# Kernel tuning notes

Measured on AMD Instinct MI355X. Metric: run time of the kernel, lower is better.

The kernel has to match this reference:

```python
import jax, jax.numpy as jnp
import numpy as np

C = 128
NUM_GROUPS = 32
EPS = 1e-6


def setup_inputs() -> dict:
    key = jax.random.key(0)
    ks = jax.random.split(key, 6)
    B, H, W = 8, 64, 64
    x = jax.random.normal(ks[0], (B, C, H, W), dtype=jnp.float32)
    # 1x1 conv weights stored as [out_c, in_c] (kernel spatial dims are 1)
    fan_avg = C  # fan_in == fan_out == C for 1x1 conv
    bound = np.sqrt(3.0 / fan_avg)
    wq = jax.random.uniform(ks[1], (C, C), jnp.float32, -bound, bound)
    wk = jax.random.uniform(ks[2], (C, C), jnp.float32, -bound, bound)
    wv = jax.random.uniform(ks[3], (C, C), jnp.float32, -bound, bound)
    # proj_out has init_scale=0.0 -> near-zero init; use tiny random instead to test math
    wo = jax.random.uniform(ks[4], (C, C), jnp.float32, -bound, bound) * 1e-3
    bq = jnp.zeros((C,), jnp.float32)
    bk = jnp.zeros((C,), jnp.float32)
    bv = jnp.zeros((C,), jnp.float32)
    bo = jnp.zeros((C,), jnp.float32)
    gamma = jnp.ones((C,), jnp.float32)
    beta = jnp.zeros((C,), jnp.float32)
    return {"x": x, "gamma": gamma, "beta": beta,
            "wq": wq, "bq": bq, "wk": wk, "bk": bk,
            "wv": wv, "bv": bv, "wo": wo, "bo": bo}


def _group_norm(x, gamma, beta):
    B, Ch, H, W = x.shape
    g = NUM_GROUPS
    xg = x.reshape(B, g, Ch // g, H, W)
    mean = jnp.mean(xg, axis=(2, 3, 4), keepdims=True)
    var = jnp.var(xg, axis=(2, 3, 4), keepdims=True)
    xn = ((xg - mean) * jax.lax.rsqrt(var + EPS)).reshape(B, Ch, H, W)
    return xn * gamma[None, :, None, None] + beta[None, :, None, None]


def _conv1x1(x, w, b):
    # x: [B,C,H,W], w: [O,C], b: [O]
    return jnp.einsum('bchw,oc->bohw', x, w) + b[None, :, None, None]


def reference(x, gamma, beta, wq, bq, wk, bk, wv, bv, wo, bo):
    B, Ch, H, W = x.shape
    n = H * W
    h = _group_norm(x, gamma, beta)
    q = _conv1x1(h, wq, bq).reshape(B, Ch, n)
    k = _conv1x1(h, wk, bk).reshape(B, Ch, n)
    v = _conv1x1(h, wv, bv).reshape(B, Ch, n)
    # attn[b, i, j] = sum_c q[b,c,i] * k[b,c,j] / sqrt(C)
    attn = jnp.einsum('bci,bcj->bij', q, k) * (float(Ch) ** -0.5)
    attn = jax.nn.softmax(attn, axis=-1)
    # h[b,c,i] = sum_j v[b,c,j] * attn[b,i,j]
    out = jnp.einsum('bcj,bij->bci', v, attn).reshape(B, Ch, H, W)
    out = _conv1x1(out, wo, bo)
    return x + out
```

## Files before the change

### kernel.cpp

```cpp
#include <hip/hip_runtime.h>


typedef float f32x4 __attribute__((ext_vector_type(4)));
typedef float f32x2 __attribute__((ext_vector_type(2)));
typedef short short8 __attribute__((ext_vector_type(8)));
typedef _Float16 half8 __attribute__((ext_vector_type(8)));
typedef _Float16 half2t __attribute__((ext_vector_type(2)));
typedef unsigned short ush;
typedef unsigned short ush4 __attribute__((ext_vector_type(4)));
typedef unsigned int uint4t __attribute__((ext_vector_type(4)));
typedef int int8v __attribute__((ext_vector_type(8)));
typedef unsigned long long ull;

union V8U {
  uint4t h[2];
  int8v v;
};

__device__ __forceinline__ ush f2bf(float f) {
  unsigned u = __builtin_bit_cast(unsigned, f);
  u = (u + 0x7FFFu + ((u >> 16) & 1u)) >> 16;
  return (ush)u;
}
__device__ __forceinline__ void async16(const void* g, void* l) {
  __builtin_amdgcn_global_load_lds(
      (const __attribute__((address_space(1))) unsigned int*)g,
      (__attribute__((address_space(3))) unsigned int*)l, 16, 0, 0);
}

__global__ __launch_bounds__(256) void gn_stats_kernel(
    const float* __restrict__ x, const float* __restrict__ gamma,
    const float* __restrict__ beta, const float* __restrict__ wo,
    const float* __restrict__ wq, const float* __restrict__ wk,
    const float* __restrict__ wv, float* __restrict__ scale_c,
    float* __restrict__ shift_c, ush* __restrict__ wobh,
    ush* __restrict__ wqh, ush* __restrict__ wkh, ush* __restrict__ wvh) {
  int bg = blockIdx.x;
  int b = bg >> 5, g = bg & 31;
  int tid = threadIdx.x;
  if (bg < 64) {
    int m = bg >> 4;
    int v4 = ((bg & 15) * 256 + tid) * 4;
    const float* src = m == 0 ? wo : (m == 1 ? wq : (m == 2 ? wk : wv));
    float4 w4 = *(const float4*)(src + v4);
    ush4 pk;
    pk.x = __builtin_bit_cast(ush, (_Float16)w4.x);
    pk.y = __builtin_bit_cast(ush, (_Float16)w4.y);
    pk.z = __builtin_bit_cast(ush, (_Float16)w4.z);
    pk.w = __builtin_bit_cast(ush, (_Float16)w4.w);
    ush* dst = m == 0 ? wobh : (m == 1 ? wqh : (m == 2 ? wkh : wvh));
    *(ush4*)(dst + v4) = pk;
  }
  const float4* base = (const float4*)(x + (size_t)bg * 16384);
  float s = 0.f, sq = 0.f;
#pragma unroll
  for (int p = 0; p < 16; ++p) {
    float4 v = base[p * 256 + tid];
    s += (v.x + v.y) + (v.z + v.w);
    sq += (v.x * v.x + v.y * v.y) + (v.z * v.z + v.w * v.w);
  }
#pragma unroll
  for (int off = 32; off > 0; off >>= 1) {
    s += __shfl_down(s, off);
    sq += __shfl_down(sq, off);
  }
  __shared__ float rs[4], rq[4], mv[2];
  int w = tid >> 6, lane = tid & 63;
  if (lane == 0) { rs[w] = s; rq[w] = sq; }
  __syncthreads();
  if (tid == 0) {
    float S = (rs[0] + rs[1]) + (rs[2] + rs[3]);
    float Q = (rq[0] + rq[1]) + (rq[2] + rq[3]);
    float mean = S * (1.f / 16384.f);
    float var = Q * (1.f / 16384.f) - mean * mean;
    mv[0] = mean;
    mv[1] = rsqrtf(var + 1e-6f);
  }
  __syncthreads();
  if (tid < 4) {
    int c = (g << 2) + tid;
    float sc = mv[1] * gamma[c];
    scale_c[(b << 7) + c] = sc;
    shift_c[(b << 7) + c] = beta[c] - mv[0] * sc;
  }
}

__global__ __launch_bounds__(256) void qkv_kernel(
    const float* __restrict__ x, const float* __restrict__ scale_c,
    const float* __restrict__ shift_c, const ush* __restrict__ wqh,
    const ush* __restrict__ wkh, const ush* __restrict__ wvh,
    const float* __restrict__ bq, const float* __restrict__ bk,
    const float* __restrict__ bv, char* __restrict__ Qt8,
    char* __restrict__ Kt8, _Float16* __restrict__ Vh) {
  __shared__ __align__(16) ush hs[64 * 136];
  __shared__ __align__(16) ush wol[128 * 136];
  char* hs8 = (char*)hs;
  int bx = blockIdx.x;
  int type = bx >> 9;
  int rb = bx & 511;
  int b = rb >> 6, i0 = (rb & 63) << 6;
  int tid = threadIdx.x;
  int w = tid >> 6, lane = tid & 63, ln15 = lane & 15, quad = lane >> 4;

#pragma unroll
  for (int p = 0; p < 8; ++p) {
    int id = p * 256 + tid;
    int i = id & 63;
    int g8 = id >> 6;
    int c0 = g8 << 2;
    const float* xp = x + (((size_t)((b << 7) + c0)) << 12) + i0 + i;
    float h0 = xp[0] * scale_c[(b << 7) + c0] + shift_c[(b << 7) + c0];
    float h1 = xp[(size_t)1 << 12] * scale_c[(b << 7) + c0 + 1] +
               shift_c[(b << 7) + c0 + 1];
    float h2 = xp[(size_t)2 << 12] * scale_c[(b << 7) + c0 + 2] +
               shift_c[(b << 7) + c0 + 2];
    float h3 = xp[(size_t)3 << 12] * scale_c[(b << 7) + c0 + 3] +
               shift_c[(b << 7) + c0 + 3];
    uint2 pk2;
    pk2.x = __builtin_bit_cast(unsigned, __builtin_amdgcn_cvt_pkrtz(h0, h1));
    pk2.y = __builtin_bit_cast(unsigned, __builtin_amdgcn_cvt_pkrtz(h2, h3));
    int pg = g8 ^ ((i & 15) << 1);
    *(uint2*)(hs8 + i * 272 + pg * 8) = pk2;
  }
  const ush* Wb = type == 0 ? wqh : (type == 1 ? wkh : wvh);
#pragma unroll
  for (int p = 0; p < 8; ++p) {
    int cid = p * 256 + tid;
    int o = cid >> 4, ch = (cid & 15) << 3;
    *(uint4t*)&wol[o * 136 + ch] = *(const uint4t*)(Wb + (o << 7) + ch);
  }
  __syncthreads();

#define HS_FRAG(row, dc)                                     \
  __builtin_bit_cast(half8, *(const short8*)(hs8 + (row) * 272 + \
      (((((dc)*4 + quad)) ^ ((row)&15)) << 4)))
#define W_FRAG(o, dc)                                         \
  __builtin_bit_cast(half8, *(const short8*)&wol[(o)*136 + (dc)*32 + quad * 8])

  if (type < 2) {
    f32x4 acc[8] = {};
    int hrow = w * 16 + ln15;
#pragma unroll
    for (int dc = 0; dc < 4; ++dc) {
      half8 af = HS_FRAG(hrow, dc);
#pragma unroll
      for (int nb = 0; nb < 8; ++nb) {
        half8 bf = W_FRAG(nb * 16 + ln15, dc);
        acc[nb] = __builtin_amdgcn_mfma_f32_16x16x32_f16(af, bf, acc[nb], 0, 0, 0);
      }
    }
    const float* bias = type == 0 ? bq : bk;
    char* dst8 = type == 0 ? Qt8 : Kt8;
    __syncthreads();
#pragma unroll
    for (int nb = 0; nb < 8; ++nb) {
      int o = nb * 16 + ln15;
      float bi = bias[o];
      float v0 = acc[nb][0] + bi, v1 = acc[nb][1] + bi;
      float v2 = acc[nb][2] + bi, v3 = acc[nb][3] + bi;
      if (type == 0) {
        v0 *= 0.12751742f; v1 *= 0.12751742f;
        v2 *= 0.12751742f; v3 *= 0.12751742f;
      }
      unsigned u = (unsigned)__builtin_amdgcn_cvt_pk_fp8_f32(v0, v1, 0, false);
      u = (unsigned)__builtin_amdgcn_cvt_pk_fp8_f32(v2, v3, (int)u, true);
      int rbase = (w * 16 + quad * 4) * 144 + o;
      hs8[rbase] = (char)(u & 0xffu);
      hs8[rbase + 144] = (char)((u >> 8) & 0xffu);
      hs8[rbase + 288] = (char)((u >> 16) & 0xffu);
      hs8[rbase + 432] = (char)(u >> 24);
    }
    __syncthreads();
    int i = tid >> 2, seg = tid & 3;
    uint4 d0 = *(const uint4*)(hs8 + i * 144 + seg * 32);
    uint4 d1 = *(const uint4*)(hs8 + i * 144 + seg * 32 + 16);
    char* drow = dst8 + (((size_t)((b << 12) + i0 + i)) << 7) + seg * 32;
    *(uint4*)drow = d0;
    *(uint4*)(drow + 16) = d1;
  } else {
    f32x4 acc[8] = {};
    int hrow = w * 16 + ln15;
#pragma unroll
    for (int dc = 0; dc < 4; ++dc) {
      half8 bf = HS_FRAG(hrow, dc);
#pragma unroll
      for (int mb = 0; mb < 8; ++mb) {
        half8 af = W_FRAG(mb * 16 + ln15, dc);
        acc[mb] = __builtin_amdgcn_mfma_f32_16x16x32_f16(af, bf, acc[mb], 0, 0, 0);
      }
    }
#pragma unroll
    for (int mb = 0; mb < 8; ++mb) {
#pragma unroll
      for (int r = 0; r < 4; ++r) {
        int o = mb * 16 + quad * 4 + r;
        float val = acc[mb][r] + bv[o];
        Vh[(((size_t)((b << 7) + o)) << 12) + i0 + w * 16 + ln15] = (_Float16)val;
      }
    }
  }
#undef HS_FRAG
#undef W_FRAG
}

__global__ __launch_bounds__(256, 2) void attn_kernel(
    const char* __restrict__ Qt8, const char* __restrict__ Kt8,
    const _Float16* __restrict__ Vh, char* __restrict__ po,
    float* __restrict__ lw) {
  __shared__ __align__(16) char ksb[2][4096];
  __shared__ __align__(16) _Float16 vsb[2][4096];
  int bx = blockIdx.x;
  int b = bx & 7, qt = (bx >> 3) & 15, ksid = bx >> 7;
  int tid = threadIdx.x;
  int w = tid >> 6, lane = tid & 63, ln15 = lane & 15, quad = lane >> 4;
  int qbase = (qt << 8) + (w << 6);
  int j0 = ksid << 10;

  int8v qf[4];
#pragma unroll
  for (int ih = 0; ih < 4; ++ih) {
    const char* qrow =
        Qt8 + (((size_t)((b << 12) + qbase + ih * 16 + ln15)) << 7) + quad * 32;
    V8U u;
    u.h[0] = *(const uint4t*)(qrow);
    u.h[1] = *(const uint4t*)(qrow + 16);
    qf[ih] = u.v;
  }

  int kj = (w << 3) + (lane >> 3);
  int kh = (kj & 3) | (((kj >> 3) & 1) << 2);
  int kg = (lane & 7) ^ kh;
  const char* ksrc = Kt8 + (((size_t)((b << 12) + j0 + kj)) << 7) + (kg << 4);
  int d0r = (w << 5) + (lane >> 2);
  int d1r = d0r + 16;
  int vg0 = (lane & 3) ^ (((d0r >> 1) + (d0r >> 3)) & 3);
  int vg1 = (lane & 3) ^ (((d1r >> 1) + (d1r >> 3)) & 3);
  const _Float16* vsrc0 =
      Vh + (((size_t)((b << 7) + d0r)) << 12) + j0 + (vg0 << 3);
  const _Float16* vsrc1 =
      Vh + (((size_t)((b << 7) + d1r)) << 12) + j0 + (vg1 << 3);
  char* kdA = &ksb[0][0] + (w << 10);
  char* kdB = &ksb[1][0] + (w << 10);
  char* vdA0 = (char*)&vsb[0][0] + ((w * 2 + 0) << 10);
  char* vdA1 = (char*)&vsb[0][0] + ((w * 2 + 1) << 10);
  char* vdB0 = (char*)&vsb[1][0] + ((w * 2 + 0) << 10);
  char* vdB1 = (char*)&vsb[1][0] + ((w * 2 + 1) << 10);

  async16(ksrc, kdA);
  async16(vsrc0, vdA0);
  async16(vsrc1, vdA1);
  __syncthreads();

  f32x4 O[4][8] = {};
  float lsum[4] = {0.f, 0.f, 0.f, 0.f};
  const f32x4 SINIT = {-7.2134752f, -7.2134752f, -7.2134752f, -7.2134752f};
  int r0 = ((ln15 >> 2) << 3) + (ln15 & 3), r1 = r0 + 4;
  int hr = (ln15 & 3) | (((ln15 >> 2) & 1) << 2);
  int g0 = ((2 * quad) ^ hr) << 4;
  int g1 = ((2 * quad + 1) ^ hr) << 4;

  for (int jt = 0; jt < 32; ++jt) {
    int buf = jt & 1;
    if (jt + 1 < 32) {
      ksrc += 4096;
      vsrc0 += 32;
      vsrc1 += 32;
      if (buf == 0) {
        async16(ksrc, kdB);
        async16(vsrc0, vdB0);
        async16(vsrc1, vdB1);
      } else {
        async16(ksrc, kdA);
        async16(vsrc0, vdA0);
        async16(vsrc1, vdA1);
      }
    }
    const char* kb = &ksb[buf][0];
    const char* vb = (const char*)&vsb[buf][0];

    V8U ka, kc;
    ka.h[0] = *(const uint4t*)(kb + r0 * 128 + g0);
    ka.h[1] = *(const uint4t*)(kb + r0 * 128 + g1);
    kc.h[0] = *(const uint4t*)(kb + r1 * 128 + g0);
    kc.h[1] = *(const uint4t*)(kb + r1 * 128 + g1);
    f32x4 S[4][2];
#pragma unroll
    for (int ih = 0; ih < 4; ++ih) {
      S[ih][0] = __builtin_amdgcn_mfma_scale_f32_16x16x128_f8f6f4(
          ka.v, qf[ih], SINIT, 0, 0, 0, 0x7F7F7F7F, 0, 0x7F7F7F7F);
      S[ih][1] = __builtin_amdgcn_mfma_scale_f32_16x16x128_f8f6f4(
          kc.v, qf[ih], SINIT, 0, 0, 0, 0x7F7F7F7F, 0, 0x7F7F7F7F);
    }

    half8 pf[4];
#pragma unroll
    for (int ih = 0; ih < 4; ++ih) {
      float p0 = __builtin_amdgcn_exp2f(S[ih][0][0]);
      float p1 = __builtin_amdgcn_exp2f(S[ih][0][1]);
      float p2 = __builtin_amdgcn_exp2f(S[ih][0][2]);
      float p3 = __builtin_amdgcn_exp2f(S[ih][0][3]);
      float p4 = __builtin_amdgcn_exp2f(S[ih][1][0]);
      float p5 = __builtin_amdgcn_exp2f(S[ih][1][1]);
      float p6 = __builtin_amdgcn_exp2f(S[ih][1][2]);
      float p7 = __builtin_amdgcn_exp2f(S[ih][1][3]);
      lsum[ih] += ((p0 + p1) + (p2 + p3)) + ((p4 + p5) + (p6 + p7));
      uint4t pw;
      pw.x = __builtin_bit_cast(unsigned, __builtin_amdgcn_cvt_pkrtz(p0, p1));
      pw.y = __builtin_bit_cast(unsigned, __builtin_amdgcn_cvt_pkrtz(p2, p3));
      pw.z = __builtin_bit_cast(unsigned, __builtin_amdgcn_cvt_pkrtz(p4, p5));
      pw.w = __builtin_bit_cast(unsigned, __builtin_amdgcn_cvt_pkrtz(p6, p7));
      pf[ih] = __builtin_bit_cast(half8, pw);
    }
#pragma unroll
    for (int nb = 0; nb < 8; ++nb) {
      int d = nb * 16 + ln15;
      int sd = ((d >> 1) + (d >> 3)) & 3;
      half8 vf = *(const half8*)(vb + d * 64 + ((quad ^ sd) << 4));
#pragma unroll
      for (int ih = 0; ih < 4; ++ih)
        O[ih][nb] = __builtin_amdgcn_mfma_f32_16x16x32_f16(vf, pf[ih], O[ih][nb], 0, 0, 0);
    }
    __syncthreads();
  }

#pragma unroll
  for (int ih = 0; ih < 4; ++ih) {
    float l = lsum[ih];
    l += __shfl_xor(l, 16);
    l += __shfl_xor(l, 32);
    if (quad == 0) lw[(ksid << 15) + (b << 12) + qbase + ih * 16 + ln15] = l;
    int i = qbase + ih * 16 + ln15;
    size_t rowb = (((size_t)((ksid * 8 + b)) << 12) + i) << 7;
#pragma unroll
    for (int nb = 0; nb < 8; ++nb) {
      unsigned u = (unsigned)__builtin_amdgcn_cvt_pk_fp8_f32(
          O[ih][nb][0], O[ih][nb][1], 0, false);
      u = (unsigned)__builtin_amdgcn_cvt_pk_fp8_f32(
          O[ih][nb][2], O[ih][nb][3], (int)u, true);
      *(unsigned*)(po + rowb + nb * 16 + quad * 4) = u;
    }
  }
}

__global__ __launch_bounds__(256) void proj_kernel(
    const float* __restrict__ x, const char* __restrict__ po,
    const float* __restrict__ lw, const ush* __restrict__ wobh,
    const float* __restrict__ bo, float* __restrict__ out) {
  int bx = blockIdx.x;
  int oh = bx & 1;
  int bi = bx >> 1;
  int b = bi >> 6, i0 = (bi & 63) << 6;
  int tid = threadIdx.x;
  int w = tid >> 6, lane = tid & 63, ln15 = lane & 15, quad = lane >> 4;
  int i = i0 + w * 16 + ln15;
  float rl = 0.f;
#pragma unroll
  for (int s = 0; s < 4; ++s) rl += lw[(s << 15) + (b << 12) + i];
  float rinv = 1.f / rl;

  f32x4 acc[4] = {};
#pragma unroll
  for (int dc = 0; dc < 4; ++dc) {
    size_t base = ((size_t)i << 7) + dc * 32 + quad * 8;
    float vs0 = 0.f, vs1 = 0.f, vs2 = 0.f, vs3 = 0.f;
    float vs4 = 0.f, vs5 = 0.f, vs6 = 0.f, vs7 = 0.f;
#pragma unroll
    for (int s = 0; s < 4; ++s) {
      ull pv = *(const ull*)(po + (((size_t)(s * 8 + b)) << 19) + base);
      int lo = (int)(unsigned)pv, hi = (int)(unsigned)(pv >> 32);
      f32x2 a0 = __builtin_amdgcn_cvt_pk_f32_fp8(lo, false);
      f32x2 a1 = __builtin_amdgcn_cvt_pk_f32_fp8(lo, true);
      f32x2 a2 = __builtin_amdgcn_cvt_pk_f32_fp8(hi, false);
      f32x2 a3 = __builtin_amdgcn_cvt_pk_f32_fp8(hi, true);
      vs0 += a0.x; vs1 += a0.y; vs2 += a1.x; vs3 += a1.y;
      vs4 += a2.x; vs5 += a2.y; vs6 += a3.x; vs7 += a3.y;
    }
    uint4t pw;
    pw.x = __builtin_bit_cast(unsigned,
                              __builtin_amdgcn_cvt_pkrtz(vs0 * rinv, vs1 * rinv));
    pw.y = __builtin_bit_cast(unsigned,
                              __builtin_amdgcn_cvt_pkrtz(vs2 * rinv, vs3 * rinv));
    pw.z = __builtin_bit_cast(unsigned,
                              __builtin_amdgcn_cvt_pkrtz(vs4 * rinv, vs5 * rinv));
    pw.w = __builtin_bit_cast(unsigned,
                              __builtin_amdgcn_cvt_pkrtz(vs6 * rinv, vs7 * rinv));
    half8 bfv = __builtin_bit_cast(half8, pw);
#pragma unroll
    for (int mb = 0; mb < 4; ++mb) {
      half8 af = *(const half8*)&wobh[(((oh * 4 + mb) * 16 + ln15) << 7) +
                                      dc * 32 + quad * 8];
      acc[mb] = __builtin_amdgcn_mfma_f32_16x16x32_f16(af, bfv, acc[mb], 0, 0, 0);
    }
  }
#pragma unroll
  for (int mb = 0; mb < 4; ++mb) {
#pragma unroll
    for (int r = 0; r < 4; ++r) {
      int o = (oh * 4 + mb) * 16 + quad * 4 + r;
      size_t idx = (((size_t)(b << 7) + o) << 12) + i;
      out[idx] = x[idx] + acc[mb][r] + bo[o];
    }
  }
}

extern "C" void kernel_launch(void* const* d_in, const int* in_sizes, int n_in,
                              void* d_out, int out_size, void* d_ws,
                              size_t ws_size, hipStream_t stream) {
  const float* x = (const float*)d_in[0];
  const float* gamma = (const float*)d_in[1];
  const float* beta = (const float*)d_in[2];
  const float* wq = (const float*)d_in[3];
  const float* bq = (const float*)d_in[4];
  const float* wk = (const float*)d_in[5];
  const float* bk = (const float*)d_in[6];
  const float* wv = (const float*)d_in[7];
  const float* bv = (const float*)d_in[8];
  const float* wo = (const float*)d_in[9];
  const float* bo = (const float*)d_in[10];
  float* out = (float*)d_out;

  const size_t NE = (size_t)8 * 4096 * 128;
  char* Qt8 = (char*)d_ws;
  char* Kt8 = Qt8 + NE;
  _Float16* Vh = (_Float16*)(Kt8 + NE);
  char* po = (char*)(Vh + NE);
  float* lwp = (float*)(po + 4 * NE);
  float* scale_c = lwp + 4 * 32768;
  float* shift_c = scale_c + 1024;
  ush* wobh = (ush*)(shift_c + 1024);
  ush* wqh = wobh + 16384;
  ush* wkh = wqh + 16384;
  ush* wvh = wkh + 16384;

  gn_stats_kernel<<<256, 256, 0, stream>>>(x, gamma, beta, wo, wq, wk, wv,
                                           scale_c, shift_c, wobh, wqh, wkh,
                                           wvh);
  qkv_kernel<<<1536, 256, 0, stream>>>(x, scale_c, shift_c, wqh, wkh, wvh, bq,
                                       bk, bv, Qt8, Kt8, Vh);
  attn_kernel<<<512, 256, 0, stream>>>(Qt8, Kt8, Vh, po, lwp);
  proj_kernel<<<1024, 256, 0, stream>>>(x, po, lwp, wobh, bo, out);
}
```

Baseline: 178.4 us.

## Fuse four kernels into one persistent kernel with grid-wide atomic barriers

Merges the group-norm stats, QKV projection, attention and output projection kernels into a single 512-block persistent kernel, separated by software grid barriers built on atomic counters. The aim is to remove three kernel launch gaps and tail effects between stages. The QKV stage now does Q, K and V per block sequentially, reusing the normalized tile in LDS instead of recomputing it in three separate blocks. The proj stage now covers all output channels per block rather than splitting them over two blocks. This relies on all 512 blocks being co-resident (launch bounds of 2 blocks per CU) and adds a memset plus spin-wait overhead.

```diff
diff --git a/kernel.cpp b/kernel.cpp
--- a/kernel.cpp
+++ b/kernel.cpp
@@ -5,7 +5,6 @@
 typedef float f32x2 __attribute__((ext_vector_type(2)));
 typedef short short8 __attribute__((ext_vector_type(8)));
 typedef _Float16 half8 __attribute__((ext_vector_type(8)));
-typedef _Float16 half2t __attribute__((ext_vector_type(2)));
 typedef unsigned short ush;
 typedef unsigned short ush4 __attribute__((ext_vector_type(4)));
 typedef unsigned int uint4t __attribute__((ext_vector_type(4)));
@@ -17,30 +16,83 @@
   int8v v;
 };
 
-__device__ __forceinline__ ush f2bf(float f) {
-  unsigned u = __builtin_bit_cast(unsigned, f);
-  u = (u + 0x7FFFu + ((u >> 16) & 1u)) >> 16;
-  return (ush)u;
-}
 __device__ __forceinline__ void async16(const void* g, void* l) {
   __builtin_amdgcn_global_load_lds(
       (const __attribute__((address_space(1))) unsigned int*)g,
       (__attribute__((address_space(3))) unsigned int*)l, 16, 0, 0);
 }
 
-__global__ __launch_bounds__(256) void gn_stats_kernel(
+__device__ __forceinline__ void gbar(unsigned* cnt, int tid) {
+  __threadfence();
+  __syncthreads();
+  if (tid == 0) {
+    __hip_atomic_fetch_add(cnt, 1u, __ATOMIC_RELEASE,
+                           __HIP_MEMORY_SCOPE_AGENT);
+    int spins = 0;
+    while (__hip_atomic_load(cnt, __ATOMIC_ACQUIRE,
+                             __HIP_MEMORY_SCOPE_AGENT) < 512u &&
+           ++spins < (1 << 22)) {
+      __builtin_amdgcn_s_sleep(8);
+    }
+  }
+  __syncthreads();
+  __threadfence();
+}
+
+__global__ __launch_bounds__(256, 2) void fused_kernel(
     const float* __restrict__ x, const float* __restrict__ gamma,
-    const float* __restrict__ beta, const float* __restrict__ wo,
-    const float* __restrict__ wq, const float* __restrict__ wk,
-    const float* __restrict__ wv, float* __restrict__ scale_c,
-    float* __restrict__ shift_c, ush* __restrict__ wobh,
-    ush* __restrict__ wqh, ush* __restrict__ wkh, ush* __restrict__ wvh) {
-  int bg = blockIdx.x;
-  int b = bg >> 5, g = bg & 31;
-  int tid = threadIdx.x;
-  if (bg < 64) {
-    int m = bg >> 4;
-    int v4 = ((bg & 15) * 256 + tid) * 4;
+    const float* __restrict__ beta, const float* __restrict__ wq,
+    const float* __restrict__ bq, const float* __restrict__ wk,
+    const float* __restrict__ bk, const float* __restrict__ wv,
+    const float* __restrict__ bv, const float* __restrict__ wo,
+    const float* __restrict__ bo, float* __restrict__ out,
+    char* __restrict__ Qt8, char* __restrict__ Kt8, _Float16* __restrict__ Vh,
+    char* __restrict__ po, float* __restrict__ lw,
+    float* __restrict__ scale_c, float* __restrict__ shift_c,
+    ush* __restrict__ wobh, ush* __restrict__ wqh, ush* __restrict__ wkh,
+    ush* __restrict__ wvh, unsigned* __restrict__ bar) {
+  __shared__ __align__(16) char smem[52224];
+  int bx = blockIdx.x, tid = threadIdx.x;
+  int w = tid >> 6, lane = tid & 63, ln15 = lane & 15, quad = lane >> 4;
+
+  if (bx < 256) {
+    int bg = bx, b = bg >> 5, g = bg & 31;
+    float* rs = (float*)smem;
+    float* rq = rs + 4;
+    float* mv = rq + 4;
+    const float4* base = (const float4*)(x + (size_t)bg * 16384);
+    float s = 0.f, sq = 0.f;
+#pragma unroll
+    for (int p = 0; p < 16; ++p) {
+      float4 v = base[p * 256 + tid];
+      s += (v.x + v.y) + (v.z + v.w);
+      sq += (v.x * v.x + v.y * v.y) + (v.z * v.z + v.w * v.w);
+    }
+#pragma unroll
+    for (int off = 32; off > 0; off >>= 1) {
+      s += __shfl_down(s, off);
+      sq += __shfl_down(sq, off);
+    }
+    if (lane == 0) { rs[w] = s; rq[w] = sq; }
+    __syncthreads();
+    if (tid == 0) {
+      float S = (rs[0] + rs[1]) + (rs[2] + rs[3]);
+      float Q = (rq[0] + rq[1]) + (rq[2] + rq[3]);
+      float mean = S * (1.f / 16384.f);
+      float var = Q * (1.f / 16384.f) - mean * mean;
+      mv[0] = mean;
+      mv[1] = rsqrtf(var + 1e-6f);
+    }
+    __syncthreads();
+    if (tid < 4) {
+      int c = (g << 2) + tid;
+      float sc = mv[1] * gamma[c];
+      scale_c[(b << 7) + c] = sc;
+      shift_c[(b << 7) + c] = beta[c] - mv[0] * sc;
+    }
+  } else if (bx < 320) {
+    int u = bx - 256, m = u >> 4;
+    int v4 = ((u & 15) * 256 + tid) * 4;
     const float* src = m == 0 ? wo : (m == 1 ? wq : (m == 2 ? wk : wv));
     float4 w4 = *(const float4*)(src + v4);
     ush4 pk;
@@ -51,142 +103,303 @@
     ush* dst = m == 0 ? wobh : (m == 1 ? wqh : (m == 2 ? wkh : wvh));
     *(ush4*)(dst + v4) = pk;
   }
-  const float4* base = (const float4*)(x + (size_t)bg * 16384);
-  float s = 0.f, sq = 0.f;
-#pragma unroll
-  for (int p = 0; p < 16; ++p) {
-    float4 v = base[p * 256 + tid];
-    s += (v.x + v.y) + (v.z + v.w);
-    sq += (v.x * v.x + v.y * v.y) + (v.z * v.z + v.w * v.w);
-  }
-#pragma unroll
-  for (int off = 32; off > 0; off >>= 1) {
-    s += __shfl_down(s, off);
-    sq += __shfl_down(sq, off);
-  }
-  __shared__ float rs[4], rq[4], mv[2];
-  int w = tid >> 6, lane = tid & 63;
-  if (lane == 0) { rs[w] = s; rq[w] = sq; }
-  __syncthreads();
-  if (tid == 0) {
-    float S = (rs[0] + rs[1]) + (rs[2] + rs[3]);
-    float Q = (rq[0] + rq[1]) + (rq[2] + rq[3]);
-    float mean = S * (1.f / 16384.f);
-    float var = Q * (1.f / 16384.f) - mean * mean;
-    mv[0] = mean;
-    mv[1] = rsqrtf(var + 1e-6f);
-  }
-  __syncthreads();
-  if (tid < 4) {
-    int c = (g << 2) + tid;
-    float sc = mv[1] * gamma[c];
-    scale_c[(b << 7) + c] = sc;
-    shift_c[(b << 7) + c] = beta[c] - mv[0] * sc;
-  }
-}
-
-__global__ __launch_bounds__(256) void qkv_kernel(
-    const float* __restrict__ x, const float* __restrict__ scale_c,
-    const float* __restrict__ shift_c, const ush* __restrict__ wqh,
-    const ush* __restrict__ wkh, const ush* __restrict__ wvh,
-    const float* __restrict__ bq, const float* __restrict__ bk,
-    const float* __restrict__ bv, char* __restrict__ Qt8,
-    char* __restrict__ Kt8, _Float16* __restrict__ Vh) {
-  __shared__ __align__(16) ush hs[64 * 136];
-  __shared__ __align__(16) ush wol[128 * 136];
-  char* hs8 = (char*)hs;
-  int bx = blockIdx.x;
-  int type = bx >> 9;
-  int rb = bx & 511;
-  int b = rb >> 6, i0 = (rb & 63) << 6;
-  int tid = threadIdx.x;
-  int w = tid >> 6, lane = tid & 63, ln15 = lane & 15, quad = lane >> 4;
-
-#pragma unroll
-  for (int p = 0; p < 8; ++p) {
-    int id = p * 256 + tid;
-    int i = id & 63;
-    int g8 = id >> 6;
-    int c0 = g8 << 2;
-    const float* xp = x + (((size_t)((b << 7) + c0)) << 12) + i0 + i;
-    float h0 = xp[0] * scale_c[(b << 7) + c0] + shift_c[(b << 7) + c0];
-    float h1 = xp[(size_t)1 << 12] * scale_c[(b << 7) + c0 + 1] +
-               shift_c[(b << 7) + c0 + 1];
-    float h2 = xp[(size_t)2 << 12] * scale_c[(b << 7) + c0 + 2] +
-               shift_c[(b << 7) + c0 + 2];
-    float h3 = xp[(size_t)3 << 12] * scale_c[(b << 7) + c0 + 3] +
-               shift_c[(b << 7) + c0 + 3];
-    uint2 pk2;
-    pk2.x = __builtin_bit_cast(unsigned, __builtin_amdgcn_cvt_pkrtz(h0, h1));
-    pk2.y = __builtin_bit_cast(unsigned, __builtin_amdgcn_cvt_pkrtz(h2, h3));
-    int pg = g8 ^ ((i & 15) << 1);
-    *(uint2*)(hs8 + i * 272 + pg * 8) = pk2;
-  }
-  const ush* Wb = type == 0 ? wqh : (type == 1 ? wkh : wvh);
-#pragma unroll
-  for (int p = 0; p < 8; ++p) {
-    int cid = p * 256 + tid;
-    int o = cid >> 4, ch = (cid & 15) << 3;
-    *(uint4t*)&wol[o * 136 + ch] = *(const uint4t*)(Wb + (o << 7) + ch);
-  }
-  __syncthreads();
-
-#define HS_FRAG(row, dc)                                     \
+  gbar(bar + 0, tid);
+
+  {
+    int b = bx >> 6, i0 = (bx & 63) << 6;
+    char* hs8 = smem;
+    ush* wol = (ush*)(smem + 17408);
+    char* wolb = (char*)wol;
+
+#pragma unroll
+    for (int p = 0; p < 8; ++p) {
+      int id = p * 256 + tid;
+      int i = id & 63;
+      int g8 = id >> 6;
+      int c0 = g8 << 2;
+      const float* xp = x + (((size_t)((b << 7) + c0)) << 12) + i0 + i;
+      float h0 = xp[0] * scale_c[(b << 7) + c0] + shift_c[(b << 7) + c0];
+      float h1 = xp[(size_t)1 << 12] * scale_c[(b << 7) + c0 + 1] +
+                 shift_c[(b << 7) + c0 + 1];
+      float h2 = xp[(size_t)2 << 12] * scale_c[(b << 7) + c0 + 2] +
+                 shift_c[(b << 7) + c0 + 2];
+      float h3 = xp[(size_t)3 << 12] * scale_c[(b << 7) + c0 + 3] +
+                 shift_c[(b << 7) + c0 + 3];
+      uint2 pk2;
+      pk2.x = __builtin_bit_cast(unsigned, __builtin_amdgcn_cvt_pkrtz(h0, h1));
+      pk2.y = __builtin_bit_cast(unsigned, __builtin_amdgcn_cvt_pkrtz(h2, h3));
+      int pg = g8 ^ ((i & 15) << 1);
+      *(uint2*)(hs8 + i * 272 + pg * 8) = pk2;
+    }
+#pragma unroll
+    for (int p = 0; p < 8; ++p) {
+      int cid = p * 256 + tid;
+      int o = cid >> 4, ch = (cid & 15) << 3;
+      *(uint4t*)&wol[o * 136 + ch] = *(const uint4t*)(wqh + (o << 7) + ch);
+    }
+    __syncthreads();
+
+#define HS_FRAG(row, dc)                                         \
   __builtin_bit_cast(half8, *(const short8*)(hs8 + (row) * 272 + \
       (((((dc)*4 + quad)) ^ ((row)&15)) << 4)))
-#define W_FRAG(o, dc)                                         \
+#define W_FRAG(o, dc)                                            \
   __builtin_bit_cast(half8, *(const short8*)&wol[(o)*136 + (dc)*32 + quad * 8])
-
-  if (type < 2) {
+    int hrow = w * 16 + ln15;
+
+#pragma unroll 1
+    for (int type = 0; type < 2; ++type) {
+      f32x4 acc[8] = {};
+#pragma unroll
+      for (int dc = 0; dc < 4; ++dc) {
+        half8 af = HS_FRAG(hrow, dc);
+#pragma unroll
+        for (int nb = 0; nb < 8; ++nb) {
+          half8 bf = W_FRAG(nb * 16 + ln15, dc);
+          acc[nb] = __builtin_amdgcn_mfma_f32_16x16x32_f16(af, bf, acc[nb], 0, 0, 0);
+        }
+      }
+      const float* bias = type == 0 ? bq : bk;
+      char* dst8 = type == 0 ? Qt8 : Kt8;
+      __syncthreads();
+#pragma unroll
+      for (int nb = 0; nb < 8; ++nb) {
+        int o = nb * 16 + ln15;
+        float bi = bias[o];
+        float v0 = acc[nb][0] + bi, v1 = acc[nb][1] + bi;
+        float v2 = acc[nb][2] + bi, v3 = acc[nb][3] + bi;
+        if (type == 0) {
+          v0 *= 0.12751742f; v1 *= 0.12751742f;
+          v2 *= 0.12751742f; v3 *= 0.12751742f;
+        }
+        unsigned u = (unsigned)__builtin_amdgcn_cvt_pk_fp8_f32(v0, v1, 0, false);
+        u = (unsigned)__builtin_amdgcn_cvt_pk_fp8_f32(v2, v3, (int)u, true);
+        int rbase = (w * 16 + quad * 4) * 144 + o;
+        wolb[rbase] = (char)(u & 0xffu);
+        wolb[rbase + 144] = (char)((u >> 8) & 0xffu);
+        wolb[rbase + 288] = (char)((u >> 16) & 0xffu);
+        wolb[rbase + 432] = (char)(u >> 24);
+      }
+      __syncthreads();
+      {
+        int i = tid >> 2, seg = tid & 3;
+        uint4 d0 = *(const uint4*)(wolb + i * 144 + seg * 32);
+        uint4 d1 = *(const uint4*)(wolb + i * 144 + seg * 32 + 16);
+        char* drow = dst8 + (((size_t)((b << 12) + i0 + i)) << 7) + seg * 32;
+        *(uint4*)drow = d0;
+        *(uint4*)(drow + 16) = d1;
+      }
+      __syncthreads();
+      const ush* Wn = type == 0 ? wkh : wvh;
+#pragma unroll
+      for (int p = 0; p < 8; ++p) {
+        int cid = p * 256 + tid;
+        int o = cid >> 4, ch = (cid & 15) << 3;
+        *(uint4t*)&wol[o * 136 + ch] = *(const uint4t*)(Wn + (o << 7) + ch);
+      }
+      __syncthreads();
+    }
+    {
+      f32x4 acc[8] = {};
+#pragma unroll
+      for (int dc = 0; dc < 4; ++dc) {
+        half8 bf = HS_FRAG(hrow, dc);
+#pragma unroll
+        for (int mb = 0; mb < 8; ++mb) {
+          half8 af = W_FRAG(mb * 16 + ln15, dc);
+          acc[mb] = __builtin_amdgcn_mfma_f32_16x16x32_f16(af, bf, acc[mb], 0, 0, 0);
+        }
+      }
+#pragma unroll
+      for (int mb = 0; mb < 8; ++mb) {
+#pragma unroll
+        for (int r = 0; r < 4; ++r) {
+          int o = mb * 16 + quad * 4 + r;
+          float val = acc[mb][r] + bv[o];
+          Vh[(((size_t)((b << 7) + o)) << 12) + i0 + w * 16 + ln15] =
+              (_Float16)val;
+        }
+      }
+    }
+#undef HS_FRAG
+#undef W_FRAG
+  }
+  gbar(bar + 1, tid);
+
+  {
+    int b = bx & 7, qt = (bx >> 3) & 15, ksid = bx >> 7;
+    int qbase = (qt << 8) + (w << 6);
+    int j0 = ksid << 10;
+    char* ksbp = smem;
+    char* vsbp = smem + 8192;
+
+    int8v qf[4];
+#pragma unroll
+    for (int ih = 0; ih < 4; ++ih) {
+      const char* qrow = Qt8 +
+                         (((size_t)((b << 12) + qbase + ih * 16 + ln15)) << 7) +
+                         quad * 32;
+      V8U u;
+      u.h[0] = *(const uint4t*)(qrow);
+      u.h[1] = *(const uint4t*)(qrow + 16);
+      qf[ih] = u.v;
+    }
+
+    int kj = (w << 3) + (lane >> 3);
+    int kh = (kj & 3) | (((kj >> 3) & 1) << 2);
+    int kg = (lane & 7) ^ kh;
+    const char* ksrc = Kt8 + (((size_t)((b << 12) + j0 + kj)) << 7) + (kg << 4);
+    int d0r = (w << 5) + (lane >> 2);
+    int d1r = d0r + 16;
+    int vg0 = (lane & 3) ^ (((d0r >> 1) + (d0r >> 3)) & 3);
+    int vg1 = (lane & 3) ^ (((d1r >> 1) + (d1r >> 3)) & 3);
+    const _Float16* vsrc0 =
+        Vh + (((size_t)((b << 7) + d0r)) << 12) + j0 + (vg0 << 3);
+    const _Float16* vsrc1 =
+        Vh + (((size_t)((b << 7) + d1r)) << 12) + j0 + (vg1 << 3);
+    char* kdA = ksbp + (w << 10);
+    char* kdB = ksbp + 4096 + (w << 10);
+    char* vdA0 = vsbp + ((w * 2 + 0) << 10);
+    char* vdA1 = vsbp + ((w * 2 + 1) << 10);
+    char* vdB0 = vsbp + 8192 + ((w * 2 + 0) << 10);
+    char* vdB1 = vsbp + 8192 + ((w * 2 + 1) << 10);
+
+    async16(ksrc, kdA);
+    async16(vsrc0, vdA0);
+    async16(vsrc1, vdA1);
+    __syncthreads();
+
+    f32x4 O[4][8] = {};
+    float lsum[4] = {0.f, 0.f, 0.f, 0.f};
+    const f32x4 SINIT = {-7.2134752f, -7.2134752f, -7.2134752f, -7.2134752f};
+    int r0 = ((ln15 >> 2) << 3) + (ln15 & 3), r1 = r0 + 4;
+    int hr = (ln15 & 3) | (((ln15 >> 2) & 1) << 2);
+    int g0 = ((2 * quad) ^ hr) << 4;
+    int g1 = ((2 * quad + 1) ^ hr) << 4;
+
+    for (int jt = 0; jt < 32; ++jt) {
+      int buf = jt & 1;
+      if (jt + 1 < 32) {
+        ksrc += 4096;
+        vsrc0 += 32;
+        vsrc1 += 32;
+        if (buf == 0) {
+          async16(ksrc, kdB);
+          async16(vsrc0, vdB0);
+          async16(vsrc1, vdB1);
+        } else {
+          async16(ksrc, kdA);
+          async16(vsrc0, vdA0);
+          async16(vsrc1, vdA1);
+        }
+      }
+      const char* kb = ksbp + buf * 4096;
+      const char* vb = vsbp + buf * 8192;
+
+      V8U ka, kc;
+      ka.h[0] = *(const uint4t*)(kb + r0 * 128 + g0);
+      ka.h[1] = *(const uint4t*)(kb + r0 * 128 + g1);
+      kc.h[0] = *(const uint4t*)(kb + r1 * 128 + g0);
+      kc.h[1] = *(const uint4t*)(kb + r1 * 128 + g1);
+      f32x4 S[4][2];
+#pragma unroll
+      for (int ih = 0; ih < 4; ++ih) {
+        S[ih][0] = __builtin_amdgcn_mfma_scale_f32_16x16x128_f8f6f4(
+            ka.v, qf[ih], SINIT, 0, 0, 0, 0x7F7F7F7F, 0, 0x7F7F7F7F);
+        S[ih][1] = __builtin_amdgcn_mfma_scale_f32_16x16x128_f8f6f4(
+            kc.v, qf[ih], SINIT, 0, 0, 0, 0x7F7F7F7F, 0, 0x7F7F7F7F);
+      }
+
+      half8 pf[4];
+#pragma unroll
+      for (int ih = 0; ih < 4; ++ih) {
+        float p0 = __builtin_amdgcn_exp2f(S[ih][0][0]);
+        float p1 = __builtin_amdgcn_exp2f(S[ih][0][1]);
+        float p2 = __builtin_amdgcn_exp2f(S[ih][0][2]);
+        float p3 = __builtin_amdgcn_exp2f(S[ih][0][3]);
+        float p4 = __builtin_amdgcn_exp2f(S[ih][1][0]);
+        float p5 = __builtin_amdgcn_exp2f(S[ih][1][1]);
+        float p6 = __builtin_amdgcn_exp2f(S[ih][1][2]);
+        float p7 = __builtin_amdgcn_exp2f(S[ih][1][3]);
+        lsum[ih] += ((p0 + p1) + (p2 + p3)) + ((p4 + p5) + (p6 + p7));
+        uint4t pw;
+        pw.x = __builtin_bit_cast(unsigned, __builtin_amdgcn_cvt_pkrtz(p0, p1));
+        pw.y = __builtin_bit_cast(unsigned, __builtin_amdgcn_cvt_pkrtz(p2, p3));
+        pw.z = __builtin_bit_cast(unsigned, __builtin_amdgcn_cvt_pkrtz(p4, p5));
+        pw.w = __builtin_bit_cast(unsigned, __builtin_amdgcn_cvt_pkrtz(p6, p7));
+        pf[ih] = __builtin_bit_cast(half8, pw);
+      }
+#pragma unroll
+      for (int nb = 0; nb < 8; ++nb) {
+        int d = nb * 16 + ln15;
+        int sd = ((d >> 1) + (d >> 3)) & 3;
+        half8 vf = *(const half8*)(vb + d * 64 + ((quad ^ sd) << 4));
+#pragma unroll
+        for (int ih = 0; ih < 4; ++ih)
+          O[ih][nb] = __builtin_amdgcn_mfma_f32_16x16x32_f16(vf, pf[ih], O[ih][nb], 0, 0, 0);
+      }
+      __syncthreads();
+    }
+
+#pragma unroll
+    for (int ih = 0; ih < 4; ++ih) {
+      float l = lsum[ih];
+      l += __shfl_xor(l, 16);
+      l += __shfl_xor(l, 32);
+      if (quad == 0) lw[(ksid << 15) + (b << 12) + qbase + ih * 16 + ln15] = l;
+      int i = qbase + ih * 16 + ln15;
+      size_t rowb = (((size_t)((ksid * 8 + b)) << 12) + i) << 7;
+#pragma unroll
+      for (int nb = 0; nb < 8; ++nb) {
+        unsigned u = (unsigned)__builtin_amdgcn_cvt_pk_fp8_f32(
+            O[ih][nb][0], O[ih][nb][1], 0, false);
+        u = (unsigned)__builtin_amdgcn_cvt_pk_fp8_f32(
+            O[ih][nb][2], O[ih][nb][3], (int)u, true);
+        *(unsigned*)(po + rowb + nb * 16 + quad * 4) = u;
+      }
+    }
+  }
+  gbar(bar + 2, tid);
+
+  {
+    int b = bx >> 6, i0 = (bx & 63) << 6;
+    int i = i0 + w * 16 + ln15;
+    float rl = 0.f;
+#pragma unroll
+    for (int s = 0; s < 4; ++s) rl += lw[(s << 15) + (b << 12) + i];
+    float rinv = 1.f / rl;
+
     f32x4 acc[8] = {};
-    int hrow = w * 16 + ln15;
 #pragma unroll
     for (int dc = 0; dc < 4; ++dc) {
-      half8 af = HS_FRAG(hrow, dc);
-#pragma unroll
-      for (int nb = 0; nb < 8; ++nb) {
-        half8 bf = W_FRAG(nb * 16 + ln15, dc);
-        acc[nb] = __builtin_amdgcn_mfma_f32_16x16x32_f16(af, bf, acc[nb], 0, 0, 0);
-      }
-    }
-    const float* bias = type == 0 ? bq : bk;
-    char* dst8 = type == 0 ? Qt8 : Kt8;
-    __syncthreads();
-#pragma unroll
-    for (int nb = 0; nb < 8; ++nb) {
-      int o = nb * 16 + ln15;
-      float bi = bias[o];
-      float v0 = acc[nb][0] + bi, v1 = acc[nb][1] + bi;
-      float v2 = acc[nb][2] + bi, v3 = acc[nb][3] + bi;
-      if (type == 0) {
-        v0 *= 0.12751742f; v1 *= 0.12751742f;
-        v2 *= 0.12751742f; v3 *= 0.12751742f;
-      }
-      unsigned u = (unsigned)__builtin_amdgcn_cvt_pk_fp8_f32(v0, v1, 0, false);
-      u = (unsigned)__builtin_amdgcn_cvt_pk_fp8_f32(v2, v3, (int)u, true);
-      int rbase = (w * 16 + quad * 4) * 144 + o;
-      hs8[rbase] = (char)(u & 0xffu);
-      hs8[rbase + 144] = (char)((u >> 8) & 0xffu);
-      hs8[rbase + 288] = (char)((u >> 16) & 0xffu);
-      hs8[rbase + 432] = (char)(u >> 24);
-    }
-    __syncthreads();
-    int i = tid >> 2, seg = tid & 3;
-    uint4 d0 = *(const uint4*)(hs8 + i * 144 + seg * 32);
-    uint4 d1 = *(const uint4*)(hs8 + i * 144 + seg * 32 + 16);
-    char* drow = dst8 + (((size_t)((b << 12) + i0 + i)) << 7) + seg * 32;
-    *(uint4*)drow = d0;
-    *(uint4*)(drow + 16) = d1;
-  } else {
-    f32x4 acc[8] = {};
-    int hrow = w * 16 + ln15;
-#pragma unroll
-    for (int dc = 0; dc < 4; ++dc) {
-      half8 bf = HS_FRAG(hrow, dc);
+      size_t base = ((size_t)i << 7) + dc * 32 + quad * 8;
+      float vs0 = 0.f, vs1 = 0.f, vs2 = 0.f, vs3 = 0.f;
+      float vs4 = 0.f, vs5 = 0.f, vs6 = 0.f, vs7 = 0.f;
+#pragma unroll
+      for (int s = 0; s < 4; ++s) {
+        ull pv = *(const ull*)(po + (((size_t)(s * 8 + b)) << 19) + base);
+        int lo = (int)(unsigned)pv, hi = (int)(unsigned)(pv >> 32);
+        f32x2 a0 = __builtin_amdgcn_cvt_pk_f32_fp8(lo, false);
+        f32x2 a1 = __builtin_amdgcn_cvt_pk_f32_fp8(lo, true);
+        f32x2 a2 = __builtin_amdgcn_cvt_pk_f32_fp8(hi, false);
+        f32x2 a3 = __builtin_amdgcn_cvt_pk_f32_fp8(hi, true);
+        vs0 += a0.x; vs1 += a0.y; vs2 += a1.x; vs3 += a1.y;
+        vs4 += a2.x; vs5 += a2.y; vs6 += a3.x; vs7 += a3.y;
+      }
+      uint4t pw;
+      pw.x = __builtin_bit_cast(unsigned,
+                                __builtin_amdgcn_cvt_pkrtz(vs0 * rinv, vs1 * rinv));
+      pw.y = __builtin_bit_cast(unsigned,
+                                __builtin_amdgcn_cvt_pkrtz(vs2 * rinv, vs3 * rinv));
+      pw.z = __builtin_bit_cast(unsigned,
+                                __builtin_amdgcn_cvt_pkrtz(vs4 * rinv, vs5 * rinv));
+      pw.w = __builtin_bit_cast(unsigned,
+                                __builtin_amdgcn_cvt_pkrtz(vs6 * rinv, vs7 * rinv));
+      half8 bfv = __builtin_bit_cast(half8, pw);
 #pragma unroll
       for (int mb = 0; mb < 8; ++mb) {
-        half8 af = W_FRAG(mb * 16 + ln15, dc);
-        acc[mb] = __builtin_amdgcn_mfma_f32_16x16x32_f16(af, bf, acc[mb], 0, 0, 0);
+        half8 af = *(const half8*)&wobh[((mb * 16 + ln15) << 7) + dc * 32 +
+                                        quad * 8];
+        acc[mb] = __builtin_amdgcn_mfma_f32_16x16x32_f16(af, bfv, acc[mb], 0, 0, 0);
       }
     }
 #pragma unroll
@@ -194,211 +407,9 @@
 #pragma unroll
       for (int r = 0; r < 4; ++r) {
         int o = mb * 16 + quad * 4 + r;
-        float val = acc[mb][r] + bv[o];
-        Vh[(((size_t)((b << 7) + o)) << 12) + i0 + w * 16 + ln15] = (_Float16)val;
-      }
-    }
-  }
-#undef HS_FRAG
-#undef W_FRAG
-}
-
-__global__ __launch_bounds__(256, 2) void attn_kernel(
-    const char* __restrict__ Qt8, const char* __restrict__ Kt8,
-    const _Float16* __restrict__ Vh, char* __restrict__ po,
-    float* __restrict__ lw) {
-  __shared__ __align__(16) char ksb[2][4096];
-  __shared__ __align__(16) _Float16 vsb[2][4096];
-  int bx = blockIdx.x;
-  int b = bx & 7, qt = (bx >> 3) & 15, ksid = bx >> 7;
-  int tid = threadIdx.x;
-  int w = tid >> 6, lane = tid & 63, ln15 = lane & 15, quad = lane >> 4;
-  int qbase = (qt << 8) + (w << 6);
-  int j0 = ksid << 10;
-
-  int8v qf[4];
-#pragma unroll
-  for (int ih = 0; ih < 4; ++ih) {
-    const char* qrow =
-        Qt8 + (((size_t)((b << 12) + qbase + ih * 16 + ln15)) << 7) + quad * 32;
-    V8U u;
-    u.h[0] = *(const uint4t*)(qrow);
-    u.h[1] = *(const uint4t*)(qrow + 16);
-    qf[ih] = u.v;
-  }
-
-  int kj = (w << 3) + (lane >> 3);
-  int kh = (kj & 3) | (((kj >> 3) & 1) << 2);
-  int kg = (lane & 7) ^ kh;
-  const char* ksrc = Kt8 + (((size_t)((b << 12) + j0 + kj)) << 7) + (kg << 4);
-  int d0r = (w << 5) + (lane >> 2);
-  int d1r = d0r + 16;
-  int vg0 = (lane & 3) ^ (((d0r >> 1) + (d0r >> 3)) & 3);
-  int vg1 = (lane & 3) ^ (((d1r >> 1) + (d1r >> 3)) & 3);
-  const _Float16* vsrc0 =
-      Vh + (((size_t)((b << 7) + d0r)) << 12) + j0 + (vg0 << 3);
-  const _Float16* vsrc1 =
-      Vh + (((size_t)((b << 7) + d1r)) << 12) + j0 + (vg1 << 3);
-  char* kdA = &ksb[0][0] + (w << 10);
-  char* kdB = &ksb[1][0] + (w << 10);
-  char* vdA0 = (char*)&vsb[0][0] + ((w * 2 + 0) << 10);
-  char* vdA1 = (char*)&vsb[0][0] + ((w * 2 + 1) << 10);
-  char* vdB0 = (char*)&vsb[1][0] + ((w * 2 + 0) << 10);
-  char* vdB1 = (char*)&vsb[1][0] + ((w * 2 + 1) << 10);
-
-  async16(ksrc, kdA);
-  async16(vsrc0, vdA0);
-  async16(vsrc1, vdA1);
-  __syncthreads();
-
-  f32x4 O[4][8] = {};
-  float lsum[4] = {0.f, 0.f, 0.f, 0.f};
-  const f32x4 SINIT = {-7.2134752f, -7.2134752f, -7.2134752f, -7.2134752f};
-  int r0 = ((ln15 >> 2) << 3) + (ln15 & 3), r1 = r0 + 4;
-  int hr = (ln15 & 3) | (((ln15 >> 2) & 1) << 2);
-  int g0 = ((2 * quad) ^ hr) << 4;
-  int g1 = ((2 * quad + 1) ^ hr) << 4;
-
-  for (int jt = 0; jt < 32; ++jt) {
-    int buf = jt & 1;
-    if (jt + 1 < 32) {
-      ksrc += 4096;
-      vsrc0 += 32;
-      vsrc1 += 32;
-      if (buf == 0) {
-        async16(ksrc, kdB);
-        async16(vsrc0, vdB0);
-        async16(vsrc1, vdB1);
-      } else {
-        async16(ksrc, kdA);
-        async16(vsrc0, vdA0);
-        async16(vsrc1, vdA1);
-      }
-    }
-    const char* kb = &ksb[buf][0];
-    const char* vb = (const char*)&vsb[buf][0];
-
-    V8U ka, kc;
-    ka.h[0] = *(const uint4t*)(kb + r0 * 128 + g0);
-    ka.h[1] = *(const uint4t*)(kb + r0 * 128 + g1);
-    kc.h[0] = *(const uint4t*)(kb + r1 * 128 + g0);
-    kc.h[1] = *(const uint4t*)(kb + r1 * 128 + g1);
-    f32x4 S[4][2];
-#pragma unroll
-    for (int ih = 0; ih < 4; ++ih) {
-      S[ih][0] = __builtin_amdgcn_mfma_scale_f32_16x16x128_f8f6f4(
-          ka.v, qf[ih], SINIT, 0, 0, 0, 0x7F7F7F7F, 0, 0x7F7F7F7F);
-      S[ih][1] = __builtin_amdgcn_mfma_scale_f32_16x16x128_f8f6f4(
-          kc.v, qf[ih], SINIT, 0, 0, 0, 0x7F7F7F7F, 0, 0x7F7F7F7F);
-    }
-
-    half8 pf[4];
-#pragma unroll
-    for (int ih = 0; ih < 4; ++ih) {
-      float p0 = __builtin_amdgcn_exp2f(S[ih][0][0]);
-      float p1 = __builtin_amdgcn_exp2f(S[ih][0][1]);
-      float p2 = __builtin_amdgcn_exp2f(S[ih][0][2]);
-      float p3 = __builtin_amdgcn_exp2f(S[ih][0][3]);
-      float p4 = __builtin_amdgcn_exp2f(S[ih][1][0]);
-      float p5 = __builtin_amdgcn_exp2f(S[ih][1][1]);
-      float p6 = __builtin_amdgcn_exp2f(S[ih][1][2]);
-      float p7 = __builtin_amdgcn_exp2f(S[ih][1][3]);
-      lsum[ih] += ((p0 + p1) + (p2 + p3)) + ((p4 + p5) + (p6 + p7));
-      uint4t pw;
-      pw.x = __builtin_bit_cast(unsigned, __builtin_amdgcn_cvt_pkrtz(p0, p1));
-      pw.y = __builtin_bit_cast(unsigned, __builtin_amdgcn_cvt_pkrtz(p2, p3));
-      pw.z = __builtin_bit_cast(unsigned, __builtin_amdgcn_cvt_pkrtz(p4, p5));
-      pw.w = __builtin_bit_cast(unsigned, __builtin_amdgcn_cvt_pkrtz(p6, p7));
-      pf[ih] = __builtin_bit_cast(half8, pw);
-    }
-#pragma unroll
-    for (int nb = 0; nb < 8; ++nb) {
-      int d = nb * 16 + ln15;
-      int sd = ((d >> 1) + (d >> 3)) & 3;
-      half8 vf = *(const half8*)(vb + d * 64 + ((quad ^ sd) << 4));
-#pragma unroll
-      for (int ih = 0; ih < 4; ++ih)
-        O[ih][nb] = __builtin_amdgcn_mfma_f32_16x16x32_f16(vf, pf[ih], O[ih][nb], 0, 0, 0);
-    }
-    __syncthreads();
-  }
-
-#pragma unroll
-  for (int ih = 0; ih < 4; ++ih) {
-    float l = lsum[ih];
-    l += __shfl_xor(l, 16);
-    l += __shfl_xor(l, 32);
-    if (quad == 0) lw[(ksid << 15) + (b << 12) + qbase + ih * 16 + ln15] = l;
-    int i = qbase + ih * 16 + ln15;
-    size_t rowb = (((size_t)((ksid * 8 + b)) << 12) + i) << 7;
-#pragma unroll
-    for (int nb = 0; nb < 8; ++nb) {
-      unsigned u = (unsigned)__builtin_amdgcn_cvt_pk_fp8_f32(
-          O[ih][nb][0], O[ih][nb][1], 0, false);
-      u = (unsigned)__builtin_amdgcn_cvt_pk_fp8_f32(
-          O[ih][nb][2], O[ih][nb][3], (int)u, true);
-      *(unsigned*)(po + rowb + nb * 16 + quad * 4) = u;
-    }
-  }
-}
-
-__global__ __launch_bounds__(256) void proj_kernel(
-    const float* __restrict__ x, const char* __restrict__ po,
-    const float* __restrict__ lw, const ush* __restrict__ wobh,
-    const float* __restrict__ bo, float* __restrict__ out) {
-  int bx = blockIdx.x;
-  int oh = bx & 1;
-  int bi = bx >> 1;
-  int b = bi >> 6, i0 = (bi & 63) << 6;
-  int tid = threadIdx.x;
-  int w = tid >> 6, lane = tid & 63, ln15 = lane & 15, quad = lane >> 4;
-  int i = i0 + w * 16 + ln15;
-  float rl = 0.f;
-#pragma unroll
-  for (int s = 0; s < 4; ++s) rl += lw[(s << 15) + (b << 12) + i];
-  float rinv = 1.f / rl;
-
-  f32x4 acc[4] = {};
-#pragma unroll
-  for (int dc = 0; dc < 4; ++dc) {
-    size_t base = ((size_t)i << 7) + dc * 32 + quad * 8;
-    float vs0 = 0.f, vs1 = 0.f, vs2 = 0.f, vs3 = 0.f;
-    float vs4 = 0.f, vs5 = 0.f, vs6 = 0.f, vs7 = 0.f;
-#pragma unroll
-    for (int s = 0; s < 4; ++s) {
-      ull pv = *(const ull*)(po + (((size_t)(s * 8 + b)) << 19) + base);
-      int lo = (int)(unsigned)pv, hi = (int)(unsigned)(pv >> 32);
-      f32x2 a0 = __builtin_amdgcn_cvt_pk_f32_fp8(lo, false);
-      f32x2 a1 = __builtin_amdgcn_cvt_pk_f32_fp8(lo, true);
-      f32x2 a2 = __builtin_amdgcn_cvt_pk_f32_fp8(hi, false);
-      f32x2 a3 = __builtin_amdgcn_cvt_pk_f32_fp8(hi, true);
-      vs0 += a0.x; vs1 += a0.y; vs2 += a1.x; vs3 += a1.y;
-      vs4 += a2.x; vs5 += a2.y; vs6 += a3.x; vs7 += a3.y;
-    }
-    uint4t pw;
-    pw.x = __builtin_bit_cast(unsigned,
-                              __builtin_amdgcn_cvt_pkrtz(vs0 * rinv, vs1 * rinv));
-    pw.y = __builtin_bit_cast(unsigned,
-                              __builtin_amdgcn_cvt_pkrtz(vs2 * rinv, vs3 * rinv));
-    pw.z = __builtin_bit_cast(unsigned,
-                              __builtin_amdgcn_cvt_pkrtz(vs4 * rinv, vs5 * rinv));
-    pw.w = __builtin_bit_cast(unsigned,
-                              __builtin_amdgcn_cvt_pkrtz(vs6 * rinv, vs7 * rinv));
-    half8 bfv = __builtin_bit_cast(half8, pw);
-#pragma unroll
-    for (int mb = 0; mb < 4; ++mb) {
-      half8 af = *(const half8*)&wobh[(((oh * 4 + mb) * 16 + ln15) << 7) +
-                                      dc * 32 + quad * 8];
-      acc[mb] = __builtin_amdgcn_mfma_f32_16x16x32_f16(af, bfv, acc[mb], 0, 0, 0);
-    }
-  }
-#pragma unroll
-  for (int mb = 0; mb < 4; ++mb) {
-#pragma unroll
-    for (int r = 0; r < 4; ++r) {
-      int o = (oh * 4 + mb) * 16 + quad * 4 + r;
-      size_t idx = (((size_t)(b << 7) + o) << 12) + i;
-      out[idx] = x[idx] + acc[mb][r] + bo[o];
+        size_t idx = (((size_t)(b << 7) + o) << 12) + i;
+        out[idx] = x[idx] + acc[mb][r] + bo[o];
+      }
     }
   }
 }
@@ -431,12 +442,10 @@
   ush* wqh = wobh + 16384;
   ush* wkh = wqh + 16384;
   ush* wvh = wkh + 16384;
-
-  gn_stats_kernel<<<256, 256, 0, stream>>>(x, gamma, beta, wo, wq, wk, wv,
-                                           scale_c, shift_c, wobh, wqh, wkh,
-                                           wvh);
-  qkv_kernel<<<1536, 256, 0, stream>>>(x, scale_c, shift_c, wqh, wkh, wvh, bq,
-                                       bk, bv, Qt8, Kt8, Vh);
-  attn_kernel<<<512, 256, 0, stream>>>(Qt8, Kt8, Vh, po, lwp);
-  proj_kernel<<<1024, 256, 0, stream>>>(x, po, lwp, wobh, bo, out);
+  unsigned* bar = (unsigned*)(wvh + 16384);
+
+  hipMemsetAsync(bar, 0, 64, stream);
+  fused_kernel<<<512, 256, 0, stream>>>(
+      x, gamma, beta, wq, bq, wk, bk, wv, bv, wo, bo, out, Qt8, Kt8, Vh, po,
+      lwp, scale_c, shift_c, wobh, wqh, wkh, wvh, bar);
 }
```

New measurement: 618.0 us. 246% more time.
